# Kernel optimization log

Hardware: AMD Instinct MI355X
Metric: run time of the kernel (lower is better)

Reference implementation:

```python
import jax, jax.numpy as jnp
import numpy as np

B, KOBJ, NS, NK = 32, 100, 16, 8
EMB, FEAT, HID, OUT, COMB = 1024, 2052, 1024, 3000, 512


def _pseudo_coord(bb_centre):
    # bb_centre (B,K,2) -> polar pseudo coords (B,K,K,2) = (rho, theta)
    d = bb_centre[:, :, None, :] - bb_centre[:, None, :, :]
    rho = jnp.sqrt(d[..., 0] ** 2 + d[..., 1] ** 2)
    theta = jnp.arctan2(d[..., 0], d[..., 1])
    return jnp.stack([rho, theta], axis=-1)


def _gauss_weights(pseudo, mr, mt, pr, pt):
    # pseudo (B,K,NS,2); kernel params (NK,) -> weights (B,K,NS,NK)
    rho = pseudo[..., 0:1]
    theta = pseudo[..., 1:2]
    w_rho = jnp.exp(-0.5 * (rho - mr) ** 2 / (1e-14 + pr ** 2))
    fa = jnp.abs(theta - mt)
    sa = jnp.abs(2.0 * jnp.pi - fa)
    w_th = jnp.exp(-0.5 * jnp.minimum(fa, sa) ** 2 / (1e-14 + pt ** 2))
    w = w_rho * w_th
    w = jnp.where(jnp.isnan(w), 0.0, w)
    return w / jnp.sum(w, axis=-1, keepdims=True)  # normalise over kernels


def _graph_conv(feats, pseudo, conv_w, mr, mt, pr, pt):
    # feats (B,K,NS,F), conv_w (NK,F,out_k) -> (B,K,NK*out_k)
    w = _gauss_weights(pseudo, mr, mt, pr, pt)          # (B,K,NS,NK)
    agg = jnp.einsum('bksm,bksf->bkmf', w, feats)       # per-kernel neighbour sum
    out = jnp.einsum('bkmf,mfo->bkmo', agg, conv_w)     # per-kernel linear
    return out.reshape(out.shape[0], out.shape[1], -1)  # kernel-major concat


def _neighbourhood(feats, pseudo, adj, weight):
    # topk over adjacency rows; softmax over topk values (== the per-row loop softmax)
    top_v, top_i = jax.lax.top_k(adj, NS)               # (B,K,NS)
    a = jax.nn.softmax(top_v, axis=-1)
    nb_f = jax.vmap(lambda f, i: f[i])(feats, top_i)    # (B,K,NS,F)
    nb_p = jnp.take_along_axis(pseudo, top_i[..., None], axis=2)  # (B,K,NS,2)
    if weight:
        nb_f = a[..., None] * nb_f
    return nb_f, nb_p


def _forward(question, image, K, W_lproj, b_lproj, W_e1, b_e1, W_e2, b_e2,
             conv_w1, mean_rho1, mean_theta1, prec_rho1, prec_theta1,
             conv_w2, mean_rho2, mean_theta2, prec_rho2, prec_theta2,
             W_o1, b_o1, W_o2, b_o2):
    bb = image[:, :, -4:]
    bb_size = bb[:, :, 2:] - bb[:, :, :2]
    bb_centre = bb[:, :, :2] + 0.5 * bb_size
    pseudo = _pseudo_coord(bb_centre)                   # (B,K,K,2)

    qenc = question @ W_lproj + b_lproj                 # (B,HID)
    qrep = jnp.broadcast_to(qenc[:, None, :], (image.shape[0], K, qenc.shape[-1]))
    cat = jnp.concatenate([image, qrep], axis=-1)       # (B,K,FEAT+HID)

    # GraphLearner: two relu linears then gram matrix
    h = jax.nn.relu(cat @ W_e1 + b_e1)
    h = jax.nn.relu(h @ W_e2 + b_e2)                    # (B,K,COMB)
    adj = jnp.einsum('bkc,blc->bkl', h, h)              # (B,K,K)

    nb_f, nb_p = _neighbourhood(image, pseudo, adj, weight=True)
    g1 = jax.nn.relu(_graph_conv(nb_f, nb_p, conv_w1, mean_rho1, mean_theta1, prec_rho1, prec_theta1))
    nb_f2, nb_p2 = _neighbourhood(g1, pseudo, adj, weight=False)
    g2 = jax.nn.relu(_graph_conv(nb_f2, nb_p2, conv_w2, mean_rho2, mean_theta2, prec_rho2, prec_theta2))
    g2 = jnp.max(g2, axis=1)                            # (B,HID)

    hh = jax.nn.relu(qenc) * g2
    h1 = jax.nn.relu(hh @ W_o1 + b_o1)
    logits = h1 @ W_o2 + b_o2
    return logits, adj


def setup_inputs() -> dict:
    key = jax.random.key(0)
    ks = jax.random.split(key, 17)
    s = jnp.float32(0.02)
    f32 = jnp.float32
    inp = {
        'question': jax.random.normal(ks[0], (B, EMB), f32),
        'image': jax.random.uniform(ks[1], (B, KOBJ, FEAT), f32),
        'K': KOBJ,
        'W_lproj': jax.random.normal(ks[2], (EMB, HID), f32) * s,
        'b_lproj': jnp.zeros((HID,), f32),
        'W_e1': jax.random.normal(ks[3], (FEAT + HID, COMB), f32) * s,
        'b_e1': jnp.zeros((COMB,), f32),
        'W_e2': jax.random.normal(ks[4], (COMB, COMB), f32) * s,
        'b_e2': jnp.zeros((COMB,), f32),
        'conv_w1': jax.random.normal(ks[5], (NK, FEAT, 2 * HID // NK), f32) * s,
        'mean_rho1': jax.random.uniform(ks[6], (NK,), f32),
        'mean_theta1': jax.random.uniform(ks[7], (NK,), f32, -np.pi, np.pi),
        'prec_rho1': jax.random.uniform(ks[8], (NK,), f32),
        'prec_theta1': jax.random.uniform(ks[9], (NK,), f32),
        'conv_w2': jax.random.normal(ks[10], (NK, 2 * HID, HID // NK), f32) * s,
        'mean_rho2': jax.random.uniform(ks[11], (NK,), f32),
        'mean_theta2': jax.random.uniform(ks[12], (NK,), f32, -np.pi, np.pi),
        'prec_rho2': jax.random.uniform(ks[13], (NK,), f32),
        'prec_theta2': jax.random.uniform(ks[14], (NK,), f32),
        'W_o1': jax.random.normal(ks[15], (HID, OUT), f32) * s,
        'b_o1': jnp.zeros((OUT,), f32),
        'W_o2': jax.random.normal(ks[16], (OUT, OUT), f32) * s,
        'b_o2': jnp.zeros((OUT,), f32),
    }
    return inp


def reference(question, image, K, W_lproj, b_lproj, W_e1, b_e1, W_e2, b_e2,
              conv_w1, mean_rho1, mean_theta1, prec_rho1, prec_theta1,
              conv_w2, mean_rho2, mean_theta2, prec_rho2, prec_theta2,
              W_o1, b_o1, W_o2, b_o2):
    return _forward(question, image, K, W_lproj, b_lproj, W_e1, b_e1, W_e2, b_e2,
                    conv_w1, mean_rho1, mean_theta1, prec_rho1, prec_theta1,
                    conv_w2, mean_rho2, mean_theta2, prec_rho2, prec_theta2,
                    W_o1, b_o1, W_o2, b_o2)
```

## Files before the change

### kernel.cpp

```cpp
#include <hip/hip_runtime.h>
#include <math.h>
#include <stdint.h>

#define B_    32
#define KOBJ  100
#define NS_   16
#define NK_   8
#define EMB_  1024
#define FEAT_ 2052
#define HID_  1024
#define OUT_  3000
#define COMB_ 512

#define KP1   2112
#define KP2   2048
#define NO_P  3072
#define KO2   3008

typedef __attribute__((ext_vector_type(8))) short s16x8;
typedef __attribute__((ext_vector_type(4))) float f32x4;

__device__ inline short f2bf(float f) {
  uint32_t u = __builtin_bit_cast(uint32_t, f);
  u = (u + 0x7fff + ((u >> 16) & 1)) >> 16;
  return (short)u;
}
__device__ inline float bf2f(short s) {
  uint32_t u = ((uint32_t)(uint16_t)s) << 16;
  return __builtin_bit_cast(float, u);
}
__device__ inline void gload_lds16(const void* g, void* l) {
  __builtin_amdgcn_global_load_lds(
      (const __attribute__((address_space(1))) void*)g,
      (__attribute__((address_space(3))) void*)l, 16, 0, 0);
}
__device__ inline int xcd_remap(int fid, int nwg) {
  int q = nwg >> 3, r = nwg & 7;
  int x = fid & 7, l = fid >> 3;
  return (x < r ? x * (q + 1) : r * (q + 1) + (x - r) * q) + l;
}

#define IMG_CHUNKS (B_ * KOBJ * (KP1 / 8))
#define IMG_BLKS   ((IMG_CHUNKS + 255) / 256)
#define Q_CHUNKS   (B_ * (EMB_ / 8))
#define Q_BLKS     ((Q_CHUNKS + 255) / 256)
#define C_BLKS     ((B_ * KOBJ + 255) / 256)

__device__ inline void cvt8_split(const float* __restrict__ in, short* __restrict__ oh,
                                  short* __restrict__ ol, int K, int Kp, int idx) {
  int row = idx / (Kp / 8), c8 = (idx % (Kp / 8)) * 8;
  float f[8];
  if (c8 + 8 <= K) {
    const float* src = in + (size_t)row * K + c8;
    float4 a = *(const float4*)src;
    float4 b = *(const float4*)(src + 4);
    f[0] = a.x; f[1] = a.y; f[2] = a.z; f[3] = a.w;
    f[4] = b.x; f[5] = b.y; f[6] = b.z; f[7] = b.w;
  } else {
#pragma unroll
    for (int i = 0; i < 8; ++i) {
      int k = c8 + i;
      f[i] = (k < K) ? in[(size_t)row * K + k] : 0.f;
    }
  }
  s16x8 vh, vl;
#pragma unroll
  for (int i = 0; i < 8; ++i) {
    short h = f2bf(f[i]);
    vh[i] = h;
    vl[i] = f2bf(f[i] - bf2f(h));
  }
  *(s16x8*)(oh + (size_t)row * Kp + c8) = vh;
  *(s16x8*)(ol + (size_t)row * Kp + c8) = vl;
}

__global__ __launch_bounds__(256) void prep_inputs(
    const float* __restrict__ image, const float* __restrict__ question,
    short* __restrict__ imgb, short* __restrict__ imgl,
    short* __restrict__ qh, short* __restrict__ ql, float* __restrict__ cent) {
  int bb = blockIdx.x, tid = threadIdx.x;
  if (bb < IMG_BLKS) {
    int idx = bb * 256 + tid;
    if (idx < IMG_CHUNKS) cvt8_split(image, imgb, imgl, FEAT_, KP1, idx);
  } else if (bb < IMG_BLKS + Q_BLKS) {
    int idx = (bb - IMG_BLKS) * 256 + tid;
    if (idx < Q_CHUNKS) cvt8_split(question, qh, ql, EMB_, EMB_, idx);
  } else {
    int i = (bb - IMG_BLKS - Q_BLKS) * 256 + tid;
    if (i < B_ * KOBJ) {
      const float* bbx = image + (size_t)i * FEAT_ + (FEAT_ - 4);
      cent[i * 2 + 0] = 0.5f * (bbx[0] + bbx[2]);
      cent[i * 2 + 1] = 0.5f * (bbx[1] + bbx[3]);
    }
  }
}

struct TD {
  const float* in; short* oh; short* ol;
  int K, N, Kp, OPM, nkt, split, conv, cum;
};
struct TDs { TD d[8]; };

__global__ __launch_bounds__(256) void transpose_all(TDs ds) {
  __shared__ float s[64][65];
  int bid = blockIdx.x;
  int i = 0;
  while (i < 7 && bid >= ds.d[i].cum) ++i;
  const TD& d = ds.d[i];
  int local = bid - (i ? ds.d[i - 1].cum : 0);
  int k0 = (local % d.nkt) * 64, n0 = (local / d.nkt) * 64;
  int t = threadIdx.x;
  int rr = t >> 4, c4 = (t & 15) * 4;
  bool fullN = d.conv || (n0 + 64 <= d.N);
#pragma unroll
  for (int p = 0; p < 4; ++p) {
    int row = p * 16 + rr;
    int kg = k0 + row;
    float v0 = 0.f, v1 = 0.f, v2 = 0.f, v3 = 0.f;
    if (kg < d.K) {
      const float* src = d.conv
          ? d.in + ((size_t)(n0 / d.OPM) * d.K + kg) * d.OPM + (n0 % d.OPM) + c4
          : d.in + (size_t)kg * d.N + n0 + c4;
      if (fullN) {
        float4 v = *(const float4*)src;
        v0 = v.x; v1 = v.y; v2 = v.z; v3 = v.w;
      } else {
        int nb = n0 + c4;
        if (nb + 0 < d.N) v0 = src[0];
        if (nb + 1 < d.N) v1 = src[1];
        if (nb + 2 < d.N) v2 = src[2];
        if (nb + 3 < d.N) v3 = src[3];
      }
    }
    s[row][c4 + 0] = v0; s[row][c4 + 1] = v1;
    s[row][c4 + 2] = v2; s[row][c4 + 3] = v3;
  }
  __syncthreads();
  int nl = t >> 2, kc = (t & 3) << 4;
#pragma unroll
  for (int half = 0; half < 2; ++half) {
    s16x8 vh, vl;
#pragma unroll
    for (int j = 0; j < 8; ++j) {
      float f = s[kc + half * 8 + j][nl];
      short h = f2bf(f);
      vh[j] = h;
      vl[j] = f2bf(f - bf2f(h));
    }
    size_t o = (size_t)(n0 + nl) * d.Kp + k0 + kc + half * 8;
    *(s16x8*)(d.oh + o) = vh;
    if (d.split) *(s16x8*)(d.ol + o) = vl;
  }
}

template <int BM, int BN, int WR, int WC, bool SPLIT, bool RELU, bool BIAS, int OMODE,
          bool SPLITK, bool PB16>
__global__ __launch_bounds__(WR * WC * 64) void gemm_mx(
    const short* __restrict__ Ah, const short* __restrict__ Al,
    const short* __restrict__ Bh, const short* __restrict__ Bl,
    const float* __restrict__ bias,
    float* __restrict__ Cf, short* __restrict__ Ch, short* __restrict__ Cl,
    float* __restrict__ part, short* __restrict__ partb, int KS,
    int M, int N, int Kp, int ldc, int Nw) {
  constexpr int NWV = WR * WC;
  constexpr int WM = BM / WR, WN = BN / WC;
  constexpr int FM = WM / 16, FN = WN / 16;
  constexpr int ACH = BM / 8, BCH = BN / 8;
  constexpr int NCH = (ACH + BCH) * (SPLIT ? 2 : 1);
  __shared__ short Ash[BM * 64];
  __shared__ short Bsh[BN * 64];
  __shared__ short Asl[SPLIT ? BM * 64 : 64];
  __shared__ short Bsl[SPLIT ? BN * 64 : 64];
  int tid = threadIdx.x, wave = tid >> 6, lane = tid & 63;
  int wr = wave / WC, wc = wave % WC;
  int r16 = lane & 15, kq = lane >> 4;
  int gx = gridDim.x, gy = gridDim.y, gz = gridDim.z;
  int fid = (blockIdx.z * gy + blockIdx.y) * gx + blockIdx.x;
  int wg = xcd_remap(fid, gx * gy * gz);
  int bx = wg % gx, byz = wg / gx;
  int by = byz % gy, bz = byz / gy;
  int m0 = by * BM, n0 = bx * BN;
  int kb = SPLITK ? bz * KS : 0;
  int ke = SPLITK ? (kb + KS < Kp ? kb + KS : Kp) : Kp;
  f32x4 acc[FM][FN] = {};

  for (int k0 = kb; k0 < ke; k0 += 64) {
    __syncthreads();
    for (int c = wave; c < NCH; c += NWV) {
      int cc = c;
      const short* g;
      char* l;
      bool isA;
      if (cc < ACH) { isA = true; g = Ah; l = (char*)Ash; }
      else if (SPLIT && cc < 2 * ACH) { cc -= ACH; isA = true; g = Al; l = (char*)Asl; }
      else {
        cc -= SPLIT ? 2 * ACH : ACH;
        if (cc < BCH) { isA = false; g = Bh; l = (char*)Bsh; }
        else { cc -= BCH; isA = false; g = Bl; l = (char*)Bsl; }
      }
      int Lb = cc * 1024 + lane * 16;
      int row = Lb >> 7;
      int off = (Lb & 127) ^ ((row & 7) << 4);
      const short* gsrc = g + (size_t)((isA ? m0 : n0) + row) * Kp + k0 + (off >> 1);
      gload_lds16(gsrc, l + cc * 1024);
    }
    __syncthreads();
#pragma unroll
    for (int kk = 0; kk < 2; ++kk) {
      int woff = kk * 64 + kq * 16;
      s16x8 ah[FM], al[FM], bh[FN], bl[FN];
#pragma unroll
      for (int f = 0; f < FM; ++f) {
        int row = wr * WM + f * 16 + r16;
        int o = woff ^ ((row & 7) << 4);
        ah[f] = *(const s16x8*)((const char*)Ash + row * 128 + o);
        if (SPLIT) al[f] = *(const s16x8*)((const char*)Asl + row * 128 + o);
      }
#pragma unroll
      for (int gg = 0; gg < FN; ++gg) {
        int row = wc * WN + gg * 16 + r16;
        int o = woff ^ ((row & 7) << 4);
        bh[gg] = *(const s16x8*)((const char*)Bsh + row * 128 + o);
        if (SPLIT) bl[gg] = *(const s16x8*)((const char*)Bsl + row * 128 + o);
      }
#pragma unroll
      for (int f = 0; f < FM; ++f)
#pragma unroll
        for (int gg = 0; gg < FN; ++gg) {
          acc[f][gg] = __builtin_amdgcn_mfma_f32_16x16x32_bf16(ah[f], bh[gg], acc[f][gg], 0, 0, 0);
          if (SPLIT) {
            acc[f][gg] = __builtin_amdgcn_mfma_f32_16x16x32_bf16(ah[f], bl[gg], acc[f][gg], 0, 0, 0);
            acc[f][gg] = __builtin_amdgcn_mfma_f32_16x16x32_bf16(al[f], bh[gg], acc[f][gg], 0, 0, 0);
          }
        }
    }
  }
#pragma unroll
  for (int f = 0; f < FM; ++f)
#pragma unroll
    for (int gg = 0; gg < FN; ++gg)
#pragma unroll
      for (int r = 0; r < 4; ++r) {
        int m = m0 + wr * WM + f * 16 + (lane >> 4) * 4 + r;
        int n = n0 + wc * WN + gg * 16 + r16;
        if (m >= M || n >= Nw) continue;
        float v = (n < N) ? acc[f][gg][r] : 0.f;
        size_t idx = (size_t)m * ldc + n;
        if (SPLITK) {
          size_t pidx = (size_t)bz * M * ldc + idx;
          if (PB16) partb[pidx] = f2bf(v);
          else      part[pidx] = v;
        } else {
          if (BIAS && n < N) v += bias[n];
          if (RELU) v = fmaxf(v, 0.f);
          if (OMODE == 0) Cf[idx] = v;
          else if (OMODE == 1) {
            short h = f2bf(v);
            Ch[idx] = h;
            Cl[idx] = f2bf(v - bf2f(h));
          } else if (OMODE == 2) {
            Ch[idx] = f2bf(v);
          } else {
            Cf[idx] = v;
            short h = f2bf(v);
            Ch[idx] = h;
            Cl[idx] = f2bf(v - bf2f(h));
          }
        }
      }
}

template <int OMODE, bool RELU, bool BIAS, bool BCAST, bool PB16>
__global__ void reduce_split(const float* __restrict__ part, const short* __restrict__ partb,
                             int SK, size_t pstride,
                             const float* __restrict__ bias, const float* __restrict__ bcast,
                             int bcols, float* __restrict__ Cf, short* __restrict__ Ch,
                             short* __restrict__ Cl, int M, int N, int ldIn, int ldOut) {
  int idx4 = blockIdx.x * 256 + threadIdx.x;
  int ld4 = ldIn >> 2;
  if (idx4 >= M * ld4) return;
  int m = idx4 / ld4;
  int n = (idx4 - m * ld4) << 2;
  size_t base = (size_t)m * ldIn + n;
  float a[4] = {0.f, 0.f, 0.f, 0.f};
  for (int s = 0; s < SK; ++s) {
    if (PB16) {
      short4 p = *(const short4*)(partb + (size_t)s * pstride + base);
      const short* pp = (const short*)&p;
#pragma unroll
      for (int j = 0; j < 4; ++j) a[j] += bf2f(pp[j]);
    } else {
      float4 p = *(const float4*)(part + (size_t)s * pstride + base);
      a[0] += p.x; a[1] += p.y; a[2] += p.z; a[3] += p.w;
    }
  }
#pragma unroll
  for (int j = 0; j < 4; ++j) {
    int nn = n + j;
    if (nn < N) {
      if (BCAST) a[j] += bcast[(size_t)(m / KOBJ) * bcols + nn];
      if (BIAS) a[j] += bias[nn];
    }
    if (RELU) a[j] = fmaxf(a[j], 0.f);
  }
  if (n >= ldOut) return;
  size_t o = (size_t)m * ldOut + n;
  if (OMODE == 0) {
    *(float4*)(Cf + o) = make_float4(a[0], a[1], a[2], a[3]);
  } else if (OMODE == 1) {
    short4 hh, ll;
    short* hp = (short*)&hh; short* lp = (short*)&ll;
#pragma unroll
    for (int j = 0; j < 4; ++j) {
      short h = f2bf(a[j]);
      hp[j] = h;
      lp[j] = f2bf(a[j] - bf2f(h));
    }
    *(short4*)(Ch + o) = hh;
    *(short4*)(Cl + o) = ll;
  } else {
    short4 hh;
    short* hp = (short*)&hh;
#pragma unroll
    for (int j = 0; j < 4; ++j) hp[j] = f2bf(a[j]);
    *(short4*)(Ch + o) = hh;
  }
}

__global__ __launch_bounds__(512) void adj_mfma(const short* __restrict__ Hh,
                                                const short* __restrict__ Hl,
                                                float* __restrict__ adj) {
  __shared__ short Ash[128 * 64];
  __shared__ short Asl[128 * 64];
  int tid = threadIdx.x, wave = tid >> 6, lane = tid & 63;
  int wr = wave >> 2, wc = wave & 3;
  int r16 = lane & 15, kq = lane >> 4;
  int b = blockIdx.x;
  const short* baseh = Hh + (size_t)b * KOBJ * COMB_;
  const short* basel = Hl + (size_t)b * KOBJ * COMB_;
  f32x4 acc[4][2] = {};
  for (int k0 = 0; k0 < COMB_; k0 += 64) {
    __syncthreads();
    for (int c = wave; c < 32; c += 8) {
      int cc = c & 15;
      bool hi = c < 16;
      int Lb = cc * 1024 + lane * 16;
      int row = Lb >> 7;
      int off = (Lb & 127) ^ ((row & 7) << 4);
      const short* gsrc = (hi ? baseh : basel) + (size_t)row * COMB_ + k0 + (off >> 1);
      gload_lds16(gsrc, (char*)(hi ? Ash : Asl) + cc * 1024);
    }
    __syncthreads();
#pragma unroll
    for (int kk = 0; kk < 2; ++kk) {
      int woff = kk * 64 + kq * 16;
      s16x8 ah[4], al[4], bh[2], bl[2];
#pragma unroll
      for (int f = 0; f < 4; ++f) {
        int row = wr * 64 + f * 16 + r16;
        int o = woff ^ ((row & 7) << 4);
        ah[f] = *(const s16x8*)((const char*)Ash + row * 128 + o);
        al[f] = *(const s16x8*)((const char*)Asl + row * 128 + o);
      }
#pragma unroll
      for (int g = 0; g < 2; ++g) {
        int row = wc * 32 + g * 16 + r16;
        int o = woff ^ ((row & 7) << 4);
        bh[g] = *(const s16x8*)((const char*)Ash + row * 128 + o);
        bl[g] = *(const s16x8*)((const char*)Asl + row * 128 + o);
      }
#pragma unroll
      for (int f = 0; f < 4; ++f)
#pragma unroll
        for (int g = 0; g < 2; ++g) {
          acc[f][g] = __builtin_amdgcn_mfma_f32_16x16x32_bf16(ah[f], bh[g], acc[f][g], 0, 0, 0);
          acc[f][g] = __builtin_amdgcn_mfma_f32_16x16x32_bf16(ah[f], bl[g], acc[f][g], 0, 0, 0);
          acc[f][g] = __builtin_amdgcn_mfma_f32_16x16x32_bf16(al[f], bh[g], acc[f][g], 0, 0, 0);
        }
    }
  }
#pragma unroll
  for (int f = 0; f < 4; ++f)
#pragma unroll
    for (int g = 0; g < 2; ++g)
#pragma unroll
      for (int r = 0; r < 4; ++r) {
        int m = wr * 64 + f * 16 + (lane >> 4) * 4 + r;
        int n = wc * 32 + g * 16 + r16;
        if (m < KOBJ && n < KOBJ)
          adj[((size_t)b * KOBJ + m) * KOBJ + n] = acc[f][g][r];
      }
}

__global__ __launch_bounds__(256) void topk_weights_kernel(
    const float* __restrict__ adj, const float* __restrict__ cent,
    const float* __restrict__ mr1, const float* __restrict__ mt1,
    const float* __restrict__ pr1, const float* __restrict__ pt1,
    const float* __restrict__ mr2, const float* __restrict__ mt2,
    const float* __restrict__ pr2, const float* __restrict__ pt2,
    int* __restrict__ topi, float* __restrict__ c1, float* __restrict__ c2) {
  int row = blockIdx.x * 4 + (threadIdx.x >> 6);
  int lane = threadIdx.x & 63;
  int b = row / KOBJ, k = row % KOBJ;
  const float* ar = adj + (size_t)row * KOBJ;
  float v0 = (lane < KOBJ) ? ar[lane] : -INFINITY;
  float v1 = (lane + 64 < KOBJ) ? ar[lane + 64] : -INFINITY;
  int i0 = lane, i1 = lane + 64;
  float tv[NS_];
  int ti[NS_];
#pragma unroll
  for (int s = 0; s < NS_; ++s) {
    bool p0 = (v0 > v1) || (v0 == v1 && i0 < i1);
    float bv = p0 ? v0 : v1;
    int bi = p0 ? i0 : i1;
#pragma unroll
    for (int off = 32; off > 0; off >>= 1) {
      float ov = __shfl_xor(bv, off);
      int oi = __shfl_xor(bi, off);
      if (ov > bv || (ov == bv && oi < bi)) { bv = ov; bi = oi; }
    }
    tv[s] = bv; ti[s] = bi;
    if (bi == i0) v0 = -INFINITY;
    if (bi == i1) v1 = -INFINITY;
  }
  float mx = tv[0], sum = 0.f, av[NS_];
#pragma unroll
  for (int s = 0; s < NS_; ++s) { av[s] = expf(tv[s] - mx); sum += av[s]; }
  if (lane < NS_) {
    int j = ti[lane];
    topi[(size_t)row * NS_ + lane] = j;
    float cx = cent[(b * KOBJ + k) * 2 + 0], cy = cent[(b * KOBJ + k) * 2 + 1];
    float dx = cx - cent[(b * KOBJ + j) * 2 + 0];
    float dy = cy - cent[(b * KOBJ + j) * 2 + 1];
    float rho = sqrtf(dx * dx + dy * dy);
    float th = atan2f(dx, dy);
    float w1[NK_], w2[NK_], s1 = 0.f, s2 = 0.f;
#pragma unroll
    for (int m = 0; m < NK_; ++m) {
      {
        float pr = pr1[m], pt = pt1[m], dr = rho - mr1[m];
        float wr = expf(-0.5f * dr * dr / (1e-14f + pr * pr));
        float fa = fabsf(th - mt1[m]);
        float sa = fabsf(6.283185307179586f - fa);
        float da = fminf(fa, sa);
        float wt = expf(-0.5f * da * da / (1e-14f + pt * pt));
        float w = wr * wt;
        if (w != w) w = 0.f;
        w1[m] = w; s1 += w;
      }
      {
        float pr = pr2[m], pt = pt2[m], dr = rho - mr2[m];
        float wr = expf(-0.5f * dr * dr / (1e-14f + pr * pr));
        float fa = fabsf(th - mt2[m]);
        float sa = fabsf(6.283185307179586f - fa);
        float da = fminf(fa, sa);
        float wt = expf(-0.5f * da * da / (1e-14f + pt * pt));
        float w = wr * wt;
        if (w != w) w = 0.f;
        w2[m] = w; s2 += w;
      }
    }
    float as = av[lane] / sum;
#pragma unroll
    for (int m = 0; m < NK_; ++m) {
      c1[((size_t)row * NS_ + lane) * NK_ + m] = as * (w1[m] / s1);
      c2[((size_t)row * NS_ + lane) * NK_ + m] = w2[m] / s2;
    }
  }
}

template <int VEC, bool BF16OUT>
__global__ __launch_bounds__(256) void combine_kernel(
    const short* __restrict__ proj, const float* __restrict__ coeff,
    const int* __restrict__ topi, float* __restrict__ outf, short* __restrict__ outb,
    int N, int mshift) {
  int row = xcd_remap(blockIdx.x, gridDim.x);
  int b = row / KOBJ;
  __shared__ int ids[NS_];
  __shared__ float cs[NS_ * NK_];
  int tid = threadIdx.x;
  if (tid < NS_) ids[tid] = topi[(size_t)row * NS_ + tid];
  else if (tid >= 32 && tid < 32 + NS_ * NK_) cs[tid - 32] = coeff[(size_t)row * NS_ * NK_ + (tid - 32)];
  __syncthreads();
  int n = tid * VEC;
  if (n >= N) return;
  int m = n >> mshift;
  float acc[VEC];
#pragma unroll
  for (int j = 0; j < VEC; ++j) acc[j] = 0.f;
#pragma unroll
  for (int s = 0; s < NS_; ++s) {
    float cc = cs[s * NK_ + m];
    const short* p = proj + ((size_t)b * KOBJ + ids[s]) * N + n;
    if (VEC == 8) {
      s16x8 v = *(const s16x8*)p;
#pragma unroll
      for (int j = 0; j < 8; ++j) acc[j] = fmaf(cc, bf2f(v[j]), acc[j]);
    } else {
      short4 v = *(const short4*)p;
      const short* vp = (const short*)&v;
#pragma unroll
      for (int j = 0; j < 4; ++j) acc[j] = fmaf(cc, bf2f(vp[j]), acc[j]);
    }
  }
#pragma unroll
  for (int j = 0; j < VEC; ++j) acc[j] = fmaxf(acc[j], 0.f);
  if (BF16OUT) {
    if (VEC == 8) {
      s16x8 o;
#pragma unroll
      for (int j = 0; j < 8; ++j) o[j] = f2bf(acc[j]);
      *(s16x8*)(outb + (size_t)row * N + n) = o;
    } else {
      short4 o;
      short* op = (short*)&o;
#pragma unroll
      for (int j = 0; j < 4; ++j) op[j] = f2bf(acc[j]);
      *(short4*)(outb + (size_t)row * N + n) = o;
    }
  } else {
    if (VEC == 4) {
      *(float4*)(outf + (size_t)row * N + n) = make_float4(acc[0], acc[1], acc[2], acc[3]);
    } else {
#pragma unroll
      for (int j = 0; j < VEC; ++j) outf[(size_t)row * N + n + j] = acc[j];
    }
  }
}

__global__ void reduce_hh_kernel(const float* __restrict__ g2, const float* __restrict__ qenc,
                                 short* __restrict__ hhb) {
  int i = blockIdx.x * blockDim.x + threadIdx.x;
  if (i >= B_ * HID_) return;
  int b = i >> 10, n = i & (HID_ - 1);
  const float* p = g2 + (size_t)b * KOBJ * HID_ + n;
  float mx = -INFINITY;
  for (int k = 0; k < KOBJ; ++k) mx = fmaxf(mx, p[(size_t)k * HID_]);
  hhb[i] = f2bf(fmaxf(qenc[i], 0.f) * mx);
}

extern "C" void kernel_launch(void* const* d_in, const int* in_sizes, int n_in,
                              void* d_out, int out_size, void* d_ws, size_t ws_size,
                              hipStream_t stream) {
  const float* question = (const float*)d_in[0];
  const float* image    = (const float*)d_in[1];
  const float* W_lproj  = (const float*)d_in[3];
  const float* b_lproj  = (const float*)d_in[4];
  const float* W_e1     = (const float*)d_in[5];
  const float* b_e1     = (const float*)d_in[6];
  const float* W_e2     = (const float*)d_in[7];
  const float* b_e2     = (const float*)d_in[8];
  const float* conv_w1  = (const float*)d_in[9];
  const float* mr1 = (const float*)d_in[10];
  const float* mt1 = (const float*)d_in[11];
  const float* pr1 = (const float*)d_in[12];
  const float* pt1 = (const float*)d_in[13];
  const float* conv_w2  = (const float*)d_in[14];
  const float* mr2 = (const float*)d_in[15];
  const float* mt2 = (const float*)d_in[16];
  const float* pr2 = (const float*)d_in[17];
  const float* pt2 = (const float*)d_in[18];
  const float* W_o1 = (const float*)d_in[19];
  const float* b_o1 = (const float*)d_in[20];
  const float* W_o2 = (const float*)d_in[21];
  const float* b_o2 = (const float*)d_in[22];

  float* out = (float*)d_out;
  float* logits = out;
  float* adj = out + B_ * OUT_;

  char* ws = (char*)d_ws;
  size_t off = 0;
  auto alloc = [&](size_t bytes) { char* p = ws + off; off += (bytes + 255) & ~((size_t)255); return p; };
  float* qenc  = (float*)alloc((size_t)B_ * HID_ * 4);
  short* qh    = (short*)alloc((size_t)B_ * EMB_ * 2);
  short* ql    = (short*)alloc((size_t)B_ * EMB_ * 2);
  short* qeh   = (short*)alloc((size_t)B_ * HID_ * 2);
  short* qel   = (short*)alloc((size_t)B_ * HID_ * 2);
  short* wlph  = (short*)alloc((size_t)EMB_ * HID_ * 2);
  short* wlpl  = (short*)alloc((size_t)EMB_ * HID_ * 2);
  short* we1ah = (short*)alloc((size_t)COMB_ * KP1 * 2);
  short* we1al = (short*)alloc((size_t)COMB_ * KP1 * 2);
  short* we1bh = (short*)alloc((size_t)COMB_ * HID_ * 2);
  short* we1bl = (short*)alloc((size_t)COMB_ * HID_ * 2);
  short* we2h  = (short*)alloc((size_t)COMB_ * COMB_ * 2);
  short* we2l  = (short*)alloc((size_t)COMB_ * COMB_ * 2);
  float* q1    = (float*)alloc((size_t)B_ * COMB_ * 4);
  short* h1h   = (short*)alloc((size_t)B_ * KOBJ * COMB_ * 2);
  short* h1l   = (short*)alloc((size_t)B_ * KOBJ * COMB_ * 2);
  short* h2h   = (short*)alloc((size_t)(B_ * KOBJ + 128) * COMB_ * 2);
  short* h2l   = (short*)alloc((size_t)(B_ * KOBJ + 128) * COMB_ * 2);
  float* cent  = (float*)alloc((size_t)B_ * KOBJ * 2 * 4);
  int*   topi  = (int*)alloc((size_t)B_ * KOBJ * NS_ * 4);
  float* c1    = (float*)alloc((size_t)B_ * KOBJ * NS_ * NK_ * 4);
  float* c2    = (float*)alloc((size_t)B_ * KOBJ * NS_ * NK_ * 4);
  short* imgb  = (short*)alloc((size_t)B_ * KOBJ * KP1 * 2);
  short* imgl  = (short*)alloc((size_t)B_ * KOBJ * KP1 * 2);
  short* cw1t  = (short*)alloc((size_t)(2 * HID_) * KP1 * 2);
  short* cw2t  = (short*)alloc((size_t)HID_ * KP2 * 2);
  short* proj1b = (short*)alloc((size_t)B_ * KOBJ * 2 * HID_ * 2);
  short* g1b   = (short*)alloc((size_t)B_ * KOBJ * KP2 * 2);
  short* proj2b = (short*)alloc((size_t)B_ * KOBJ * HID_ * 2);
  float* g2    = (float*)alloc((size_t)B_ * KOBJ * HID_ * 4);
  short* hhb   = (short*)alloc((size_t)B_ * HID_ * 2);
  short* wo1t  = (short*)alloc((size_t)NO_P * HID_ * 2);
  short* wo2t  = (short*)alloc((size_t)NO_P * KO2 * 2);
  short* h1ob  = (short*)alloc((size_t)B_ * KO2 * 2);
  float* partE = (float*)alloc((size_t)4 * B_ * KOBJ * COMB_ * 4);
  short* partS = (short*)partE;
  (void)ws_size; (void)in_sizes; (void)n_in; (void)out_size;

  dim3 blk(256), blk512(512);

  prep_inputs<<<dim3(IMG_BLKS + Q_BLKS + C_BLKS), blk, 0, stream>>>(
      image, question, imgb, imgl, qh, ql, cent);

  {
    TDs ds;
    int cum = 0;
    auto set = [&](int i, const float* in, short* oh, short* ol, int K, int N, int Kp,
                   int OPM, int nnt, int split, int conv) {
      int nkt = Kp / 64;
      cum += nkt * nnt;
      ds.d[i] = TD{in, oh, ol, K, N, Kp, OPM, nkt, split, conv, cum};
    };
    set(0, W_lproj, wlph, wlpl, EMB_, HID_, EMB_, 0, HID_ / 64, 1, 0);
    set(1, W_e1, we1ah, we1al, FEAT_, COMB_, KP1, 0, COMB_ / 64, 1, 0);
    set(2, W_e1 + (size_t)FEAT_ * COMB_, we1bh, we1bl, HID_, COMB_, HID_, 0, COMB_ / 64, 1, 0);
    set(3, W_e2, we2h, we2l, COMB_, COMB_, COMB_, 0, COMB_ / 64, 1, 0);
    set(4, conv_w1, cw1t, nullptr, FEAT_, 2 * HID_, KP1, 2 * HID_ / NK_, 2 * HID_ / 64, 0, 1);
    set(5, conv_w2, cw2t, nullptr, 2 * HID_, HID_, KP2, HID_ / NK_, HID_ / 64, 0, 1);
    set(6, W_o1, wo1t, nullptr, HID_, OUT_, HID_, 0, NO_P / 64, 0, 0);
    set(7, W_o2, wo2t, nullptr, OUT_, OUT_, KO2, 0, NO_P / 64, 0, 0);
    transpose_all<<<dim3(cum), blk, 0, stream>>>(ds);
  }

  gemm_mx<32, 64, 2, 2, true, false, true, 3, false, false><<<dim3(HID_ / 64, 1, 1), blk, 0, stream>>>(
      qh, ql, wlph, wlpl, b_lproj, qenc, qeh, qel, nullptr, nullptr, 0, B_, HID_, EMB_, HID_, HID_);
  gemm_mx<32, 64, 2, 2, true, false, false, 0, false, false><<<dim3(COMB_ / 64, 1, 1), blk, 0, stream>>>(
      qeh, qel, we1bh, we1bl, nullptr, q1, nullptr, nullptr, nullptr, nullptr, 0, B_, COMB_, HID_, COMB_, COMB_);
  gemm_mx<128, 64, 4, 2, true, false, false, 0, true, false><<<dim3(COMB_ / 64, B_ * KOBJ / 128, 4), blk512, 0, stream>>>(
      imgb, imgl, we1ah, we1al, nullptr, nullptr, nullptr, nullptr, partE, nullptr, 576,
      B_ * KOBJ, COMB_, KP1, COMB_, COMB_);
  reduce_split<1, true, true, true, false><<<dim3(B_ * KOBJ * COMB_ / 4 / 256), blk, 0, stream>>>(
      partE, nullptr, 4, (size_t)B_ * KOBJ * COMB_, b_e1, q1, COMB_, nullptr, h1h, h1l,
      B_ * KOBJ, COMB_, COMB_, COMB_);
  gemm_mx<128, 64, 4, 2, true, false, false, 0, true, false><<<dim3(COMB_ / 64, B_ * KOBJ / 128, 4), blk512, 0, stream>>>(
      h1h, h1l, we2h, we2l, nullptr, nullptr, nullptr, nullptr, partE, nullptr, 128,
      B_ * KOBJ, COMB_, COMB_, COMB_, COMB_);
  reduce_split<1, true, true, false, false><<<dim3(B_ * KOBJ * COMB_ / 4 / 256), blk, 0, stream>>>(
      partE, nullptr, 4, (size_t)B_ * KOBJ * COMB_, b_e2, nullptr, 0, nullptr, h2h, h2l,
      B_ * KOBJ, COMB_, COMB_, COMB_);
  adj_mfma<<<dim3(B_), blk512, 0, stream>>>(h2h, h2l, adj);
  topk_weights_kernel<<<dim3(B_ * KOBJ / 4), blk, 0, stream>>>(
      adj, cent, mr1, mt1, pr1, pt1, mr2, mt2, pr2, pt2, topi, c1, c2);
  gemm_mx<128, 128, 2, 4, false, false, false, 0, true, true><<<dim3(2 * HID_ / 128, B_ * KOBJ / 128, 2), blk512, 0, stream>>>(
      imgb, nullptr, cw1t, nullptr, nullptr, nullptr, nullptr, nullptr, nullptr, partS, 1056,
      B_ * KOBJ, 2 * HID_, KP1, 2 * HID_, 2 * HID_);
  reduce_split<2, false, false, false, true><<<dim3(B_ * KOBJ * 2 * HID_ / 4 / 256), blk, 0, stream>>>(
      nullptr, partS, 2, (size_t)B_ * KOBJ * 2 * HID_, nullptr, nullptr, 0, nullptr, proj1b, nullptr,
      B_ * KOBJ, 2 * HID_, 2 * HID_, 2 * HID_);
  combine_kernel<8, true><<<dim3(B_ * KOBJ), blk, 0, stream>>>(
      proj1b, c1, topi, nullptr, g1b, 2 * HID_, 8);
  gemm_mx<128, 128, 2, 4, false, false, false, 0, true, true><<<dim3(HID_ / 128, B_ * KOBJ / 128, 4), blk512, 0, stream>>>(
      g1b, nullptr, cw2t, nullptr, nullptr, nullptr, nullptr, nullptr, nullptr, partS, 512,
      B_ * KOBJ, HID_, KP2, HID_, HID_);
  reduce_split<2, false, false, false, true><<<dim3(B_ * KOBJ * HID_ / 4 / 256), blk, 0, stream>>>(
      nullptr, partS, 4, (size_t)B_ * KOBJ * HID_, nullptr, nullptr, 0, nullptr, proj2b, nullptr,
      B_ * KOBJ, HID_, HID_, HID_);
  combine_kernel<4, false><<<dim3(B_ * KOBJ), blk, 0, stream>>>(
      proj2b, c2, topi, g2, nullptr, HID_, 7);
  reduce_hh_kernel<<<dim3((B_ * HID_ + 255) / 256), blk, 0, stream>>>(g2, qenc, hhb);
  gemm_mx<32, 128, 1, 4, false, false, false, 0, true, false><<<dim3(NO_P / 128, 1, 16), blk, 0, stream>>>(
      hhb, nullptr, wo1t, nullptr, nullptr, nullptr, nullptr, nullptr, partE, nullptr, 64,
      B_, OUT_, HID_, KO2, KO2);
  reduce_split<2, true, true, false, false><<<dim3((B_ * KO2 / 4 + 255) / 256), blk, 0, stream>>>(
      partE, nullptr, 16, (size_t)B_ * KO2, b_o1, nullptr, 0, nullptr, h1ob, nullptr,
      B_, OUT_, KO2, KO2);
  gemm_mx<32, 128, 1, 4, false, false, false, 0, true, false><<<dim3(NO_P / 128, 1, 16), blk, 0, stream>>>(
      h1ob, nullptr, wo2t, nullptr, nullptr, nullptr, nullptr, nullptr, partE, nullptr, 192,
      B_, OUT_, KO2, KO2, KO2);
  reduce_split<0, false, true, false, false><<<dim3((B_ * KO2 / 4 + 255) / 256), blk, 0, stream>>>(
      partE, nullptr, 16, (size_t)B_ * KO2, b_o2, nullptr, 0, logits, nullptr, nullptr,
      B_, OUT_, KO2, OUT_);
}
```

Baseline: 345.1 us.

## Fuse E1 and proj1 split-K GEMMs into one heterogeneous launch

Refactors the GEMM into a device body taking explicit block coordinates and shared memory, then launches a single kernel whose first blocks compute the E1 partial GEMM and the rest compute the proj1 GEMM over the same image input. Both read imgb, so co-scheduling aims to share L2 traffic, drop a launch, and fill the device better than two separate grids. The proj1 partial output moves to its own buffer because it no longer aliases partE. The cost is extra workspace, and both branches now use a 48KB dynamic shared allocation that can lower occupancy for the smaller-tile branch.

New measurement: 338.8 us. About the same (-1.8%).

```diff
diff --git a/kernel.cpp b/kernel.cpp
--- a/kernel.cpp
+++ b/kernel.cpp
@@ -155,7 +155,8 @@
 
 template <int BM, int BN, int WR, int WC, bool SPLIT, bool RELU, bool BIAS, int OMODE,
           bool SPLITK, bool PB16>
-__global__ __launch_bounds__(WR * WC * 64) void gemm_mx(
+__device__ __forceinline__ void gemm_body(
+    char* smem, int bx, int by, int bz,
     const short* __restrict__ Ah, const short* __restrict__ Al,
     const short* __restrict__ Bh, const short* __restrict__ Bl,
     const float* __restrict__ bias,
@@ -167,18 +168,13 @@
   constexpr int FM = WM / 16, FN = WN / 16;
   constexpr int ACH = BM / 8, BCH = BN / 8;
   constexpr int NCH = (ACH + BCH) * (SPLIT ? 2 : 1);
-  __shared__ short Ash[BM * 64];
-  __shared__ short Bsh[BN * 64];
-  __shared__ short Asl[SPLIT ? BM * 64 : 64];
-  __shared__ short Bsl[SPLIT ? BN * 64 : 64];
+  char* AshC = smem;
+  char* BshC = smem + BM * 128;
+  char* AslC = smem + (BM + BN) * 128;
+  char* BslC = smem + (2 * BM + BN) * 128;
   int tid = threadIdx.x, wave = tid >> 6, lane = tid & 63;
   int wr = wave / WC, wc = wave % WC;
   int r16 = lane & 15, kq = lane >> 4;
-  int gx = gridDim.x, gy = gridDim.y, gz = gridDim.z;
-  int fid = (blockIdx.z * gy + blockIdx.y) * gx + blockIdx.x;
-  int wg = xcd_remap(fid, gx * gy * gz);
-  int bx = wg % gx, byz = wg / gx;
-  int by = byz % gy, bz = byz / gy;
   int m0 = by * BM, n0 = bx * BN;
   int kb = SPLITK ? bz * KS : 0;
   int ke = SPLITK ? (kb + KS < Kp ? kb + KS : Kp) : Kp;
@@ -191,12 +187,12 @@
       const short* g;
       char* l;
       bool isA;
-      if (cc < ACH) { isA = true; g = Ah; l = (char*)Ash; }
-      else if (SPLIT && cc < 2 * ACH) { cc -= ACH; isA = true; g = Al; l = (char*)Asl; }
+      if (cc < ACH) { isA = true; g = Ah; l = AshC; }
+      else if (SPLIT && cc < 2 * ACH) { cc -= ACH; isA = true; g = Al; l = AslC; }
       else {
         cc -= SPLIT ? 2 * ACH : ACH;
-        if (cc < BCH) { isA = false; g = Bh; l = (char*)Bsh; }
-        else { cc -= BCH; isA = false; g = Bl; l = (char*)Bsl; }
+        if (cc < BCH) { isA = false; g = Bh; l = BshC; }
+        else { cc -= BCH; isA = false; g = Bl; l = BslC; }
       }
       int Lb = cc * 1024 + lane * 16;
       int row = Lb >> 7;
@@ -213,15 +209,15 @@
       for (int f = 0; f < FM; ++f) {
         int row = wr * WM + f * 16 + r16;
         int o = woff ^ ((row & 7) << 4);
-        ah[f] = *(const s16x8*)((const char*)Ash + row * 128 + o);
-        if (SPLIT) al[f] = *(const s16x8*)((const char*)Asl + row * 128 + o);
+        ah[f] = *(const s16x8*)(AshC + row * 128 + o);
+        if (SPLIT) al[f] = *(const s16x8*)(AslC + row * 128 + o);
       }
 #pragma unroll
       for (int gg = 0; gg < FN; ++gg) {
         int row = wc * WN + gg * 16 + r16;
         int o = woff ^ ((row & 7) << 4);
-        bh[gg] = *(const s16x8*)((const char*)Bsh + row * 128 + o);
-        if (SPLIT) bl[gg] = *(const s16x8*)((const char*)Bsl + row * 128 + o);
+        bh[gg] = *(const s16x8*)(BshC + row * 128 + o);
+        if (SPLIT) bl[gg] = *(const s16x8*)(BslC + row * 128 + o);
       }
 #pragma unroll
       for (int f = 0; f < FM; ++f)
@@ -268,6 +264,56 @@
           }
         }
       }
+}
+
+template <int BM, int BN, int WR, int WC, bool SPLIT, bool RELU, bool BIAS, int OMODE,
+          bool SPLITK, bool PB16>
+__global__ __launch_bounds__(WR * WC * 64) void gemm_mx(
+    const short* __restrict__ Ah, const short* __restrict__ Al,
+    const short* __restrict__ Bh, const short* __restrict__ Bl,
+    const float* __restrict__ bias,
+    float* __restrict__ Cf, short* __restrict__ Ch, short* __restrict__ Cl,
+    float* __restrict__ part, short* __restrict__ partb, int KS,
+    int M, int N, int Kp, int ldc, int Nw) {
+  __shared__ char smem_s[(BM + BN) * 128 * (SPLIT ? 2 : 1)];
+  int gx = gridDim.x, gy = gridDim.y, gz = gridDim.z;
+  int fid = (blockIdx.z * gy + blockIdx.y) * gx + blockIdx.x;
+  int wg = xcd_remap(fid, gx * gy * gz);
+  int bx = wg % gx, byz = wg / gx;
+  int by = byz % gy, bz = byz / gy;
+  gemm_body<BM, BN, WR, WC, SPLIT, RELU, BIAS, OMODE, SPLITK, PB16>(
+      smem_s, bx, by, bz, Ah, Al, Bh, Bl, bias, Cf, Ch, Cl, part, partb, KS,
+      M, N, Kp, ldc, Nw);
+}
+
+#define E1B 800
+#define P1B 800
+__global__ __launch_bounds__(512) void fused_e1_proj1(
+    const short* __restrict__ imgb, const short* __restrict__ imgl,
+    const short* __restrict__ we1ah, const short* __restrict__ we1al,
+    float* __restrict__ partE,
+    const short* __restrict__ cw1t, short* __restrict__ partP) {
+  extern __shared__ char smem[];
+  int fid = blockIdx.x;
+  if (fid < E1B) {
+    int wg = xcd_remap(fid, E1B);
+    int gx = COMB_ / 64;
+    int bx = wg % gx, t = wg / gx;
+    int by = t % (B_ * KOBJ / 128), bz = t / (B_ * KOBJ / 128);
+    gemm_body<128, 64, 4, 2, true, false, false, 0, true, false>(
+        smem, bx, by, bz, imgb, imgl, we1ah, we1al, nullptr,
+        nullptr, nullptr, nullptr, partE, nullptr, 576,
+        B_ * KOBJ, COMB_, KP1, COMB_, COMB_);
+  } else {
+    int wg = xcd_remap(fid - E1B, P1B);
+    int gx = 2 * HID_ / 128;
+    int bx = wg % gx, t = wg / gx;
+    int by = t % (B_ * KOBJ / 128), bz = t / (B_ * KOBJ / 128);
+    gemm_body<128, 128, 2, 4, false, false, false, 0, true, true>(
+        smem, bx, by, bz, imgb, nullptr, cw1t, nullptr, nullptr,
+        nullptr, nullptr, nullptr, nullptr, partP, 1056,
+        B_ * KOBJ, 2 * HID_, KP1, 2 * HID_, 2 * HID_);
+  }
 }
 
 template <int OMODE, bool RELU, bool BIAS, bool BCAST, bool PB16>
@@ -607,7 +653,7 @@
   short* wo2t  = (short*)alloc((size_t)NO_P * KO2 * 2);
   short* h1ob  = (short*)alloc((size_t)B_ * KO2 * 2);
   float* partE = (float*)alloc((size_t)4 * B_ * KOBJ * COMB_ * 4);
-  short* partS = (short*)partE;
+  short* partP = (short*)alloc((size_t)2 * B_ * KOBJ * 2 * HID_ * 2);
   (void)ws_size; (void)in_sizes; (void)n_in; (void)out_size;
 
   dim3 blk(256), blk512(512);
@@ -639,9 +685,8 @@
       qh, ql, wlph, wlpl, b_lproj, qenc, qeh, qel, nullptr, nullptr, 0, B_, HID_, EMB_, HID_, HID_);
   gemm_mx<32, 64, 2, 2, true, false, false, 0, false, false><<<dim3(COMB_ / 64, 1, 1), blk, 0, stream>>>(
       qeh, qel, we1bh, we1bl, nullptr, q1, nullptr, nullptr, nullptr, nullptr, 0, B_, COMB_, HID_, COMB_, COMB_);
-  gemm_mx<128, 64, 4, 2, true, false, false, 0, true, false><<<dim3(COMB_ / 64, B_ * KOBJ / 128, 4), blk512, 0, stream>>>(
-      imgb, imgl, we1ah, we1al, nullptr, nullptr, nullptr, nullptr, partE, nullptr, 576,
-      B_ * KOBJ, COMB_, KP1, COMB_, COMB_);
+  fused_e1_proj1<<<dim3(E1B + P1B), blk512, 49152, stream>>>(
+      imgb, imgl, we1ah, we1al, partE, cw1t, partP);
   reduce_split<1, true, true, true, false><<<dim3(B_ * KOBJ * COMB_ / 4 / 256), blk, 0, stream>>>(
       partE, nullptr, 4, (size_t)B_ * KOBJ * COMB_, b_e1, q1, COMB_, nullptr, h1h, h1l,
       B_ * KOBJ, COMB_, COMB_, COMB_);
@@ -654,19 +699,16 @@
   adj_mfma<<<dim3(B_), blk512, 0, stream>>>(h2h, h2l, adj);
   topk_weights_kernel<<<dim3(B_ * KOBJ / 4), blk, 0, stream>>>(
       adj, cent, mr1, mt1, pr1, pt1, mr2, mt2, pr2, pt2, topi, c1, c2);
-  gemm_mx<128, 128, 2, 4, false, false, false, 0, true, true><<<dim3(2 * HID_ / 128, B_ * KOBJ / 128, 2), blk512, 0, stream>>>(
-      imgb, nullptr, cw1t, nullptr, nullptr, nullptr, nullptr, nullptr, nullptr, partS, 1056,
-      B_ * KOBJ, 2 * HID_, KP1, 2 * HID_, 2 * HID_);
   reduce_split<2, false, false, false, true><<<dim3(B_ * KOBJ * 2 * HID_ / 4 / 256), blk, 0, stream>>>(
-      nullptr, partS, 2, (size_t)B_ * KOBJ * 2 * HID_, nullptr, nullptr, 0, nullptr, proj1b, nullptr,
+      nullptr, partP, 2, (size_t)B_ * KOBJ * 2 * HID_, nullptr, nullptr, 0, nullptr, proj1b, nullptr,
       B_ * KOBJ, 2 * HID_, 2 * HID_, 2 * HID_);
   combine_kernel<8, true><<<dim3(B_ * KOBJ), blk, 0, stream>>>(
       proj1b, c1, topi, nullptr, g1b, 2 * HID_, 8);
   gemm_mx<128, 128, 2, 4, false, false, false, 0, true, true><<<dim3(HID_ / 128, B_ * KOBJ / 128, 4), blk512, 0, stream>>>(
-      g1b, nullptr, cw2t, nullptr, nullptr, nullptr, nullptr, nullptr, nullptr, partS, 512,
+      g1b, nullptr, cw2t, nullptr, nullptr, nullptr, nullptr, nullptr, nullptr, partP, 512,
       B_ * KOBJ, HID_, KP2, HID_, HID_);
   reduce_split<2, false, false, false, true><<<dim3(B_ * KOBJ * HID_ / 4 / 256), blk, 0, stream>>>(
-      nullptr, partS, 4, (size_t)B_ * KOBJ * HID_, nullptr, nullptr, 0, nullptr, proj2b, nullptr,
+      nullptr, partP, 4, (size_t)B_ * KOBJ * HID_, nullptr, nullptr, 0, nullptr, proj2b, nullptr,
       B_ * KOBJ, HID_, HID_, HID_);
   combine_kernel<4, false><<<dim3(B_ * KOBJ), blk, 0, stream>>>(
       proj2b, c2, topi, g2, nullptr, HID_, 7);
```
